# Kernel tuning notes

Measured on AMD Instinct MI355X. Metric: run time of the kernel, lower is better.

The kernel has to match this reference:

```python
import jax, jax.numpy as jnp
import numpy as np

T, D, H = 2048, 1024, 16
HS = D // H  # head_size = 64
DFF = 4 * D
LN_EPS = 1e-6


def layernorm(x, scale, bias, eps=LN_EPS):
    mu = jnp.mean(x, axis=-1, keepdims=True)
    var = jnp.mean(jnp.square(x - mu), axis=-1, keepdims=True)
    return (x - mu) * jax.lax.rsqrt(var + eps) * scale + bias


def setup_inputs() -> dict:
    key = jax.random.key(0)
    ks = jax.random.split(key, 12)
    s_in = 1.0 / np.sqrt(D)
    s_ff = 1.0 / np.sqrt(DFF)
    return {
        "x": jax.random.normal(ks[0], (T, D), jnp.float32),
        "Wq": jax.random.normal(ks[1], (H, D, HS), jnp.float32) * s_in,
        "Wk": jax.random.normal(ks[2], (H, D, HS), jnp.float32) * s_in,
        "Wv": jax.random.normal(ks[3], (H, D, HS), jnp.float32) * s_in,
        "Wo": jax.random.normal(ks[4], (D, D), jnp.float32) * s_in,
        "bo": jnp.zeros((D,), jnp.float32),
        "W1": jax.random.normal(ks[5], (D, DFF), jnp.float32) * s_in,
        "b1": jnp.zeros((DFF,), jnp.float32),
        "W2": jax.random.normal(ks[6], (DFF, D), jnp.float32) * s_ff,
        "b2": jnp.zeros((D,), jnp.float32),
        "ln1_scale": jnp.ones((D,), jnp.float32),
        "ln1_bias": jnp.zeros((D,), jnp.float32),
        "ln2_scale": jnp.ones((D,), jnp.float32),
        "ln2_bias": jnp.zeros((D,), jnp.float32),
        "training": 0,
    }


def reference(x, Wq, Wk, Wv, Wo, bo, W1, b1, W2, b2,
              ln1_scale, ln1_bias, ln2_scale, ln2_bias, training):
    # --- pre-LN causal multi-head self-attention ---
    h = layernorm(x, ln1_scale, ln1_bias)
    q = jnp.einsum("td,hdk->htk", h, Wq)  # [H,T,HS]
    k = jnp.einsum("td,hdk->htk", h, Wk)
    v = jnp.einsum("td,hdk->htk", h, Wv)
    scores = jnp.einsum("htk,hsk->hts", q, k) / jnp.sqrt(jnp.float32(HS))
    causal = jnp.tril(jnp.ones((T, T), jnp.float32))
    scores = jnp.where(causal == 0, -jnp.inf, scores)
    wei = jax.nn.softmax(scores, axis=-1)
    av = jnp.einsum("hts,hsk->htk", wei, v)          # [H,T,HS]
    av = av.transpose(1, 0, 2).reshape(T, H * HS)    # concat over heads
    x = x + av @ Wo + bo                              # dropout deterministic -> identity
    # --- pre-LN feed-forward ---
    h2 = layernorm(x, ln2_scale, ln2_bias)
    ff = jax.nn.relu(h2 @ W1 + b1) @ W2 + b2
    x = x + ff
    return x
```

## Files before the change

### kernel.cpp

```cpp
#include <hip/hip_runtime.h>
#include <cstdint>


typedef __bf16 bf16;
typedef __bf16 bf16x4 __attribute__((ext_vector_type(4)));
typedef __bf16 bf16x8 __attribute__((ext_vector_type(8)));
typedef float floatx4 __attribute__((ext_vector_type(4)));

__device__ __forceinline__ void ld_g2l(const bf16* g, bf16* l) {
    __builtin_amdgcn_global_load_lds(
        (const __attribute__((address_space(1))) void*)g,
        (__attribute__((address_space(3))) void*)l, 16, 0, 0);
}

__device__ __forceinline__ void ln_row_body(
    const float* __restrict__ x, const float* __restrict__ sc,
    const float* __restrict__ bi, bf16* __restrict__ out,
    int row, int tid, float* wred)
{
    const float4 v = ((const float4*)(x + (size_t)row * 1024))[tid];
    float s1 = v.x + v.y + v.z + v.w;
    float s2 = v.x * v.x + v.y * v.y + v.z * v.z + v.w * v.w;
#pragma unroll
    for (int mm = 1; mm < 64; mm <<= 1) {
        s1 += __shfl_xor(s1, mm);
        s2 += __shfl_xor(s2, mm);
    }
    const int wave = tid >> 6, lane = tid & 63;
    if (lane == 0) { wred[wave] = s1; wred[4 + wave] = s2; }
    __syncthreads();
    s1 = wred[0] + wred[1] + wred[2] + wred[3];
    s2 = wred[4] + wred[5] + wred[6] + wred[7];
    const float mu = s1 * (1.f / 1024.f);
    const float var = fmaxf(s2 * (1.f / 1024.f) - mu * mu, 0.f);
    const float rr = rsqrtf(var + 1e-6f);
    const float4 scv = ((const float4*)sc)[tid];
    const float4 biv = ((const float4*)bi)[tid];
    bf16x4 ov;
    ov[0] = (bf16)((v.x - mu) * rr * scv.x + biv.x);
    ov[1] = (bf16)((v.y - mu) * rr * scv.y + biv.y);
    ov[2] = (bf16)((v.z - mu) * rr * scv.z + biv.z);
    ov[3] = (bf16)((v.w - mu) * rr * scv.w + biv.w);
    *(bf16x4*)(out + (size_t)row * 1024 + tid * 4) = ov;
}

__global__ __launch_bounds__(256) void prep_kernel(
    const float* __restrict__ Wq, const float* __restrict__ Wk,
    const float* __restrict__ Wv, bf16* __restrict__ Wqkvt,
    const float* __restrict__ Wo, bf16* __restrict__ Wot,
    const float* __restrict__ W1, bf16* __restrict__ W1t,
    const float* __restrict__ W2, bf16* __restrict__ W2t,
    const float* __restrict__ x, const float* __restrict__ ln1s,
    const float* __restrict__ ln1b, bf16* __restrict__ hbuf)
{
    __shared__ float tile[64][65];
    __shared__ float wred[8];
    const int b = blockIdx.x;
    const int tid = threadIdx.x;

    if (b >= 3072) {
        ln_row_body(x, ln1s, ln1b, hbuf, b - 3072, tid, wred);
        return;
    }

    const int tx = tid & 63, ty = tid >> 6;
    const float* src; bf16* dst; int R, C, c0, r0;
    if (b < 768) {
        const int sec = b >> 4, ti = b & 15;
        const int m = sec >> 4, h = sec & 15;
        src = (m == 0 ? Wq : (m == 1 ? Wk : Wv)) + h * 65536;
        dst = Wqkvt + m * 1048576 + h * 65536;
        R = 1024; C = 64; c0 = 0; r0 = ti * 64;
    } else if (b < 1024) {
        const int i = b - 768;
        src = Wo; dst = Wot; R = 1024; C = 1024;
        c0 = (i & 15) * 64; r0 = (i >> 4) * 64;
    } else if (b < 2048) {
        const int i = b - 1024;
        src = W1; dst = W1t; R = 1024; C = 4096;
        c0 = (i & 63) * 64; r0 = (i >> 6) * 64;
    } else {
        const int i = b - 2048;
        src = W2; dst = W2t; R = 4096; C = 1024;
        c0 = (i & 15) * 64; r0 = (i >> 4) * 64;
    }
#pragma unroll
    for (int i = ty; i < 64; i += 4)
        tile[i][tx] = src[(size_t)(r0 + i) * C + c0 + tx];
    __syncthreads();
#pragma unroll
    for (int i = ty; i < 64; i += 4)
        dst[(size_t)(c0 + i) * R + r0 + tx] = (bf16)tile[tx][i];
}

__global__ __launch_bounds__(256) void ln_kernel(
    const float* __restrict__ x, const float* __restrict__ sc,
    const float* __restrict__ bi, bf16* __restrict__ out)
{
    __shared__ float wred[8];
    ln_row_body(x, sc, bi, out, blockIdx.x, threadIdx.x, wred);
}

__global__ __launch_bounds__(256) void reduce4_kernel(
    const float* __restrict__ p, const float* __restrict__ bias,
    const float* __restrict__ res, float* __restrict__ out)
{
    const int idx = blockIdx.x * 256 + threadIdx.x;
    const int c4 = idx & 255;
    const float4 a0 = ((const float4*)p)[idx];
    const float4 a1 = ((const float4*)(p + 2097152))[idx];
    const float4 a2 = ((const float4*)(p + 4194304))[idx];
    const float4 a3 = ((const float4*)(p + 6291456))[idx];
    const float4 bi = ((const float4*)bias)[c4];
    const float4 r = ((const float4*)res)[idx];
    float4 o;
    o.x = (a0.x + a1.x) + (a2.x + a3.x) + bi.x + r.x;
    o.y = (a0.y + a1.y) + (a2.y + a3.y) + bi.y + r.y;
    o.z = (a0.z + a1.z) + (a2.z + a3.z) + bi.z + r.z;
    o.w = (a0.w + a1.w) + (a2.w + a3.w) + bi.w + r.w;
    ((float4*)out)[idx] = o;
}

template <int MODE, int NG, int MG, int SPLITK>
__global__ __launch_bounds__(512) void gemm128_kernel(
    const bf16* __restrict__ A, const bf16* __restrict__ Bt,
    int N, int K,
    float* __restrict__ outF, bf16* __restrict__ outB,
    const float* __restrict__ bias)
{
    __shared__ __align__(16) bf16 Alds[2][128][64];
    __shared__ __align__(16) bf16 Blds[2][128][64];
    const int tid  = threadIdx.x;
    const int lane = tid & 63;
    const int w    = tid >> 6;
    const int r15  = lane & 15;
    const int quad = lane >> 4;

    const int id    = blockIdx.x + gridDim.x * (blockIdx.y + gridDim.y * blockIdx.z);
    const int xcd   = id & 7;
    const int seq   = id >> 3;
    const int nPerX = gridDim.x / NG;
    const int mPerX = gridDim.y / MG;
    const int nm    = nPerX * mPerX;
    const int z     = seq / nm;
    const int loc   = seq - z * nm;
    const int bn    = ((xcd % NG) * nPerX + (loc % nPerX)) * 128;
    const int bm    = ((xcd / NG) * mPerX + (loc / nPerX)) * 128;

    const int wm = (w >> 2) * 64;
    const int wn = (w & 3) * 32;

    floatx4 acc[4][2];
#pragma unroll
    for (int i = 0; i < 4; ++i)
#pragma unroll
        for (int j = 0; j < 2; ++j) acc[i][j] = (floatx4)(0.f);

    const int KS    = K / SPLITK;
    const int kBase = (SPLITK > 1) ? z * KS : 0;
    const int nIter = KS / 64;

    const int lrow = lane >> 3;
    const int gch  = (lane & 7) ^ lrow;
    const bf16* aptr = A + (size_t)(bm + w * 16 + lrow) * K + kBase + gch * 8;
    const bf16* bptr = Bt + (size_t)(bn + w * 16 + lrow) * K + kBase + gch * 8;

#pragma unroll
    for (int t = 0; t < 2; ++t) {
        ld_g2l(aptr + (size_t)(t * 8) * K, &Alds[0][w * 16 + t * 8][0]);
        ld_g2l(bptr + (size_t)(t * 8) * K, &Blds[0][w * 16 + t * 8][0]);
    }

    for (int it = 0; it < nIter; ++it) {
        const int buf = it & 1;
        __syncthreads();
        if (it + 1 < nIter) {
            const int k2 = (it + 1) * 64;
#pragma unroll
            for (int t = 0; t < 2; ++t) {
                ld_g2l(aptr + (size_t)(t * 8) * K + k2, &Alds[buf ^ 1][w * 16 + t * 8][0]);
                ld_g2l(bptr + (size_t)(t * 8) * K + k2, &Blds[buf ^ 1][w * 16 + t * 8][0]);
            }
        }
#pragma unroll
        for (int kk = 0; kk < 2; ++kk) {
            const int pc = ((kk * 4 + quad) ^ (r15 & 7)) * 8;
            bf16x8 af[4], bfr[2];
#pragma unroll
            for (int i = 0; i < 4; ++i)
                af[i] = *(const bf16x8*)(&Alds[buf][wm + i * 16 + r15][pc]);
#pragma unroll
            for (int j = 0; j < 2; ++j)
                bfr[j] = *(const bf16x8*)(&Blds[buf][wn + j * 16 + r15][pc]);
#pragma unroll
            for (int i = 0; i < 4; ++i)
#pragma unroll
                for (int j = 0; j < 2; ++j)
                    acc[i][j] = __builtin_amdgcn_mfma_f32_16x16x32_bf16(
                        af[i], bfr[j], acc[i][j], 0, 0, 0);
        }
    }

    const int row0 = bm + wm + quad * 4;
    const int col0 = bn + wn + r15;

    if (MODE == 1 && bn >= 2048) {
        bf16* vt = (bf16*)outF;
#pragma unroll
        for (int i = 0; i < 4; ++i) {
            const int row = row0 + i * 16;
#pragma unroll
            for (int j = 0; j < 2; ++j) {
                const int col = col0 + j * 16 - 2048;
                bf16x4 pv;
#pragma unroll
                for (int reg = 0; reg < 4; ++reg) pv[reg] = (bf16)acc[i][j][reg];
                *(bf16x4*)(vt + (size_t)(col >> 6) * 131072
                              + (size_t)(col & 63) * 2048 + row) = pv;
            }
        }
        return;
    }

    float* po = (MODE == 3) ? outF + (size_t)z * 2048 * 1024 : outF;
#pragma unroll
    for (int i = 0; i < 4; ++i) {
#pragma unroll
        for (int reg = 0; reg < 4; ++reg) {
            const int row = row0 + i * 16 + reg;
#pragma unroll
            for (int j = 0; j < 2; ++j) {
                const int col = col0 + j * 16;
                float v = acc[i][j][reg];
                if (MODE == 0 || MODE == 1) {
                    outB[(size_t)row * N + col] = (bf16)v;
                } else if (MODE == 2) {
                    v += bias[col];
                    outB[(size_t)row * N + col] = (bf16)fmaxf(v, 0.f);
                } else {
                    po[(size_t)row * N + col] = v;
                }
            }
        }
    }
}

template <int NG, int MG>
__global__ __launch_bounds__(256) void gemm64_kernel(
    const bf16* __restrict__ A, const bf16* __restrict__ Bt,
    int N, int K,
    float* __restrict__ outF, const float* __restrict__ bias,
    const float* __restrict__ res)
{
    __shared__ __align__(16) bf16 Alds[2][64][64];
    __shared__ __align__(16) bf16 Blds[2][64][64];
    const int tid  = threadIdx.x;
    const int lane = tid & 63;
    const int w    = tid >> 6;
    const int r15  = lane & 15;
    const int quad = lane >> 4;

    const int id    = blockIdx.x + gridDim.x * blockIdx.y;
    const int xcd   = id & 7;
    const int seq   = id >> 3;
    const int nPerX = gridDim.x / NG;
    const int mPerX = gridDim.y / MG;
    const int loc   = seq % (nPerX * mPerX);
    const int bn    = ((xcd % NG) * nPerX + (loc % nPerX)) * 64;
    const int bm    = ((xcd / NG) * mPerX + (loc / nPerX)) * 64;

    const int wm = (w >> 1) * 32;
    const int wn = (w & 1) * 32;

    floatx4 acc[2][2];
#pragma unroll
    for (int i = 0; i < 2; ++i)
#pragma unroll
        for (int j = 0; j < 2; ++j) acc[i][j] = (floatx4)(0.f);

    const int nIter = K / 64;
    const int lrow = lane >> 3;
    const int gch  = (lane & 7) ^ lrow;
    const bf16* aptr = A + (size_t)(bm + w * 16 + lrow) * K + gch * 8;
    const bf16* bptr = Bt + (size_t)(bn + w * 16 + lrow) * K + gch * 8;

#pragma unroll
    for (int t = 0; t < 2; ++t) {
        ld_g2l(aptr + (size_t)t * 8 * K, &Alds[0][w * 16 + t * 8][0]);
        ld_g2l(bptr + (size_t)t * 8 * K, &Blds[0][w * 16 + t * 8][0]);
    }

    for (int it = 0; it < nIter; ++it) {
        const int buf = it & 1;
        __syncthreads();
        if (it + 1 < nIter) {
            const int k2 = (it + 1) * 64;
#pragma unroll
            for (int t = 0; t < 2; ++t) {
                ld_g2l(aptr + (size_t)t * 8 * K + k2, &Alds[buf ^ 1][w * 16 + t * 8][0]);
                ld_g2l(bptr + (size_t)t * 8 * K + k2, &Blds[buf ^ 1][w * 16 + t * 8][0]);
            }
        }
#pragma unroll
        for (int kk = 0; kk < 2; ++kk) {
            const int pc = ((kk * 4 + quad) ^ (r15 & 7)) * 8;
            bf16x8 af[2], bfr[2];
#pragma unroll
            for (int i = 0; i < 2; ++i)
                af[i] = *(const bf16x8*)(&Alds[buf][wm + i * 16 + r15][pc]);
#pragma unroll
            for (int j = 0; j < 2; ++j)
                bfr[j] = *(const bf16x8*)(&Blds[buf][wn + j * 16 + r15][pc]);
#pragma unroll
            for (int i = 0; i < 2; ++i)
#pragma unroll
                for (int j = 0; j < 2; ++j)
                    acc[i][j] = __builtin_amdgcn_mfma_f32_16x16x32_bf16(
                        af[i], bfr[j], acc[i][j], 0, 0, 0);
        }
    }

    const int row0 = bm + wm + quad * 4;
    const int col0 = bn + wn + r15;
#pragma unroll
    for (int i = 0; i < 2; ++i)
#pragma unroll
        for (int reg = 0; reg < 4; ++reg) {
            const int row = row0 + i * 16 + reg;
#pragma unroll
            for (int j = 0; j < 2; ++j) {
                const int col = col0 + j * 16;
                outF[(size_t)row * N + col] =
                    acc[i][j][reg] + bias[col] + res[(size_t)row * N + col];
            }
        }
}

__global__ __launch_bounds__(256) void attn_kernel(
    const bf16* __restrict__ qkv, const bf16* __restrict__ vt,
    bf16* __restrict__ Opart, float* __restrict__ Lpart)
{
    __shared__ __align__(16) bf16 Qs[64][64];
    __shared__ __align__(16) bf16 Ks[2][64][64];
    __shared__ __align__(16) bf16 Vs[2][64][64];
    __shared__ __align__(16) bf16 Ps[4][16][72];

    const int tid  = threadIdx.x;
    const int w    = tid >> 6;
    const int lane = tid & 63;
    const int r15  = lane & 15;
    const int quad = lane >> 4;
    const int rl   = lane >> 3;
    const int gsw  = (lane & 7) ^ (rl & 7);

    const int b    = blockIdx.x;
    const int idp  = b & 255;
    const int seq  = idp >> 3;
    const int h    = (idp & 7) * 2 + (seq & 1);
    const int qp   = seq >> 1;
    const int qt   = ((b >> 8) & 1) ? 31 - qp : qp;
    const int half = b >> 9;
    const int qrow0 = qt * 64;

    const int n0    = (qt + 2) >> 1;
    const int sbBeg = half ? n0 : 0;
    const int sbEnd = half ? qt + 1 : n0;

    if (sbBeg >= sbEnd) return;

    const int tile = half * 512 + h * 32 + qt;
    const size_t obase = (size_t)tile * 4096;

    const bf16* qsec = qkv + h * 64;
    const bf16* ksec = qkv + 1024 + h * 64;
    const bf16* vth  = vt + (size_t)h * 64 * 2048;
    const int s0 = sbBeg * 64;

#pragma unroll
    for (int t = 0; t < 2; ++t) {
        const int r = t * 32 + w * 8 + rl;
        ld_g2l(qsec + (size_t)(qrow0 + r) * 3072 + gsw * 8, &Qs[t * 32 + w * 8][0]);
        ld_g2l(ksec + (size_t)(s0 + r) * 3072 + gsw * 8, &Ks[0][t * 32 + w * 8][0]);
        ld_g2l(vth + (size_t)r * 2048 + s0 + gsw * 8, &Vs[0][t * 32 + w * 8][0]);
    }
    __syncthreads();

    bf16x8 qf[2];
#pragma unroll
    for (int c = 0; c < 2; ++c) {
        const int p = ((c * 4 + quad) ^ (r15 & 7)) * 8;
        qf[c] = *(const bf16x8*)&Qs[w * 16 + r15][p];
    }

    float lacc[4] = {0.f, 0.f, 0.f, 0.f};
    floatx4 O[4];
#pragma unroll
    for (int j = 0; j < 4; ++j) O[j] = (floatx4)(0.f);

    int ns = 0;
#pragma unroll 1
    for (int sb = sbBeg; sb < sbEnd; ++sb, ++ns) {
        const int buf = ns & 1;
        if (sb + 1 < sbEnd) {
            const int s1 = (sb + 1) * 64;
#pragma unroll
            for (int t = 0; t < 2; ++t) {
                const int r = t * 32 + w * 8 + rl;
                ld_g2l(ksec + (size_t)(s1 + r) * 3072 + gsw * 8, &Ks[buf ^ 1][t * 32 + w * 8][0]);
                ld_g2l(vth + (size_t)r * 2048 + s1 + gsw * 8, &Vs[buf ^ 1][t * 32 + w * 8][0]);
            }
        }

        floatx4 S[4];
#pragma unroll
        for (int j = 0; j < 4; ++j) S[j] = (floatx4)(0.f);
        __builtin_amdgcn_s_setprio(1);
#pragma unroll
        for (int c = 0; c < 2; ++c) {
#pragma unroll
            for (int j = 0; j < 4; ++j) {
                const int p = ((c * 4 + quad) ^ (r15 & 7)) * 8;
                const bf16x8 kb = *(const bf16x8*)&Ks[buf][j * 16 + r15][p];
                S[j] = __builtin_amdgcn_mfma_f32_16x16x32_bf16(qf[c], kb, S[j], 0, 0, 0);
            }
        }
        __builtin_amdgcn_s_setprio(0);
        if (sb == qt) {
            const int rowl = w * 16 + quad * 4;
#pragma unroll
            for (int j = 0; j < 4; ++j) {
                const int col = j * 16 + r15;
#pragma unroll
                for (int r = 0; r < 4; ++r) {
                    float p = exp2f(fmaf(S[j][r], 0.18033688f, -28.853901f));
                    if (col > rowl + r) p = 0.f;
                    S[j][r] = p;
                    lacc[r] += p;
                }
            }
        } else {
#pragma unroll
            for (int j = 0; j < 4; ++j)
#pragma unroll
                for (int r = 0; r < 4; ++r) {
                    const float p = exp2f(fmaf(S[j][r], 0.18033688f, -28.853901f));
                    S[j][r] = p;
                    lacc[r] += p;
                }
        }
#pragma unroll
        for (int r = 0; r < 4; ++r)
#pragma unroll
            for (int j = 0; j < 4; ++j)
                Ps[w][quad * 4 + r][j * 16 + r15] = (bf16)S[j][r];
        __builtin_amdgcn_s_setprio(1);
#pragma unroll
        for (int c = 0; c < 2; ++c) {
            const bf16x8 a = *(const bf16x8*)&Ps[w][r15][c * 32 + quad * 8];
#pragma unroll
            for (int j = 0; j < 4; ++j) {
                const int p = ((c * 4 + quad) ^ (r15 & 7)) * 8;
                const bf16x8 vb = *(const bf16x8*)&Vs[buf][j * 16 + r15][p];
                O[j] = __builtin_amdgcn_mfma_f32_16x16x32_bf16(a, vb, O[j], 0, 0, 0);
            }
        }
        __builtin_amdgcn_s_setprio(0);
        __syncthreads();
    }
#pragma unroll
    for (int r = 0; r < 4; ++r) {
#pragma unroll
        for (int d = 1; d < 16; d <<= 1) lacc[r] += __shfl_xor(lacc[r], d);
    }
#pragma unroll
    for (int r = 0; r < 4; ++r) {
        const int row = w * 16 + quad * 4 + r;
#pragma unroll
        for (int j = 0; j < 4; ++j)
            Opart[obase + (size_t)row * 64 + j * 16 + r15] = (bf16)(O[j][r]);
    }
    if (r15 == 0) {
#pragma unroll
        for (int r = 0; r < 4; ++r)
            Lpart[tile * 64 + w * 16 + quad * 4 + r] = lacc[r];
    }
}

__global__ __launch_bounds__(256) void attn_combine_kernel(
    const bf16* __restrict__ Op, const float* __restrict__ Lp,
    bf16* __restrict__ out)
{
    const int b = blockIdx.x;
    const int h = b >> 5, qt = b & 31;
    const int tid = threadIdx.x;
    const int r = tid >> 2, cg = tid & 3;
    const size_t pa = (size_t)b * 4096 + r * 64 + cg * 16;
    const bf16x8 a0 = *(const bf16x8*)(Op + pa);
    const bf16x8 a1 = *(const bf16x8*)(Op + pa + 8);
    const float la = Lp[b * 64 + r];
    bf16x8 o0, o1;
    if (qt > 0) {
        const bf16x8 b0 = *(const bf16x8*)(Op + 2097152 + pa);
        const bf16x8 b1 = *(const bf16x8*)(Op + 2097152 + pa + 8);
        const float lb = Lp[32768 + b * 64 + r];
        const float inv = 1.f / (la + lb);
#pragma unroll
        for (int i = 0; i < 8; ++i) {
            o0[i] = (bf16)(((float)a0[i] + (float)b0[i]) * inv);
            o1[i] = (bf16)(((float)a1[i] + (float)b1[i]) * inv);
        }
    } else {
        const float inv = 1.f / la;
#pragma unroll
        for (int i = 0; i < 8; ++i) {
            o0[i] = (bf16)((float)a0[i] * inv);
            o1[i] = (bf16)((float)a1[i] * inv);
        }
    }
    bf16* dst = out + (size_t)(qt * 64 + r) * 1024 + h * 64 + cg * 16;
    *(bf16x8*)dst = o0;
    *(bf16x8*)(dst + 8) = o1;
}

extern "C" void kernel_launch(void* const* d_in, const int* in_sizes, int n_in,
                              void* d_out, int out_size, void* d_ws, size_t ws_size,
                              hipStream_t stream)
{
    const float* x    = (const float*)d_in[0];
    const float* Wq   = (const float*)d_in[1];
    const float* Wk   = (const float*)d_in[2];
    const float* Wv   = (const float*)d_in[3];
    const float* Wo   = (const float*)d_in[4];
    const float* bo   = (const float*)d_in[5];
    const float* W1   = (const float*)d_in[6];
    const float* b1   = (const float*)d_in[7];
    const float* W2   = (const float*)d_in[8];
    const float* b2   = (const float*)d_in[9];
    const float* ln1s = (const float*)d_in[10];
    const float* ln1b = (const float*)d_in[11];
    const float* ln2s = (const float*)d_in[12];
    const float* ln2b = (const float*)d_in[13];

    char* ws = (char*)d_ws;
    bf16*  Wqkvt = (bf16*)(ws + 0);
    bf16*  Wot   = (bf16*)(ws + 6291456);
    bf16*  W1t   = (bf16*)(ws + 8388608);
    bf16*  W2t   = (bf16*)(ws + 16777216);
    bf16*  hbuf  = (bf16*)(ws + 25165824);
    bf16*  QKV   = (bf16*)(ws + 29360128);
    bf16*  Vt    = (bf16*)(ws + 41943040);
    bf16*  Obuf  = (bf16*)(ws + 46137344);
    float* x1    = (float*)(ws + 50331648);
    bf16*  h2    = (bf16*)(ws + 58720256);
    bf16*  ff1   = (bf16*)(ws + 62914560);
    float* psum  = (float*)(ws + 79691776);
    bf16*  Opart = (bf16*)(ws + 79691776);
    float* Lpart = (float*)(ws + 88080384);

    prep_kernel<<<5120, 256, 0, stream>>>(Wq, Wk, Wv, Wqkvt, Wo, Wot,
                                          W1, W1t, W2, W2t,
                                          x, ln1s, ln1b, hbuf);
    gemm128_kernel<1,4,2,1><<<dim3(24, 16), 512, 0, stream>>>(hbuf, Wqkvt, 3072, 1024, (float*)Vt, QKV, nullptr);
    attn_kernel<<<1024, 256, 0, stream>>>(QKV, Vt, Opart, Lpart);
    attn_combine_kernel<<<512, 256, 0, stream>>>(Opart, Lpart, Obuf);
    gemm64_kernel<4,2><<<dim3(16, 32), 256, 0, stream>>>(Obuf, Wot, 1024, 1024, x1, bo, x);
    ln_kernel<<<2048, 256, 0, stream>>>(x1, ln2s, ln2b, h2);
    gemm128_kernel<2,4,2,1><<<dim3(32, 16), 512, 0, stream>>>(h2, W1t, 4096, 1024, nullptr, ff1, b1);
    gemm128_kernel<3,2,4,4><<<dim3(8, 16, 4), 512, 0, stream>>>(ff1, W2t, 1024, 4096, psum, nullptr, nullptr);
    reduce4_kernel<<<2048, 256, 0, stream>>>(psum, b2, x1, (float*)d_out);
}
```

Measured before the change: 248.1 us.

## Fuse attention split combine into O-projection GEMM and store split-K partials as bf16

Removes the separate attention-combine kernel and has the O-projection GEMM load the two partial attention outputs and their normalizers directly, normalizing them in registers before writing the A tile into LDS. The next tile's partials are prefetched through registers while the current tile's MFMAs run. Separately, the FFN down-projection now writes its split-K partials as bf16 instead of fp32, halving that traffic, and the reduce kernel handles 8 elements per thread. The cost is extra register pressure and VALU work inside the GEMM loop, plus extra rounding of the partial sums before they are reduced.

```diff
diff --git a/kernel.cpp b/kernel.cpp
--- a/kernel.cpp
+++ b/kernel.cpp
@@ -102,23 +102,31 @@
 }
 
 __global__ __launch_bounds__(256) void reduce4_kernel(
-    const float* __restrict__ p, const float* __restrict__ bias,
+    const bf16* __restrict__ p, const float* __restrict__ bias,
     const float* __restrict__ res, float* __restrict__ out)
 {
     const int idx = blockIdx.x * 256 + threadIdx.x;
-    const int c4 = idx & 255;
-    const float4 a0 = ((const float4*)p)[idx];
-    const float4 a1 = ((const float4*)(p + 2097152))[idx];
-    const float4 a2 = ((const float4*)(p + 4194304))[idx];
-    const float4 a3 = ((const float4*)(p + 6291456))[idx];
-    const float4 bi = ((const float4*)bias)[c4];
-    const float4 r = ((const float4*)res)[idx];
-    float4 o;
-    o.x = (a0.x + a1.x) + (a2.x + a3.x) + bi.x + r.x;
-    o.y = (a0.y + a1.y) + (a2.y + a3.y) + bi.y + r.y;
-    o.z = (a0.z + a1.z) + (a2.z + a3.z) + bi.z + r.z;
-    o.w = (a0.w + a1.w) + (a2.w + a3.w) + bi.w + r.w;
-    ((float4*)out)[idx] = o;
+    const size_t e = (size_t)idx * 8;
+    const int c = (int)(e & 1023);
+    const bf16x8 a0 = *(const bf16x8*)(p + e);
+    const bf16x8 a1 = *(const bf16x8*)(p + 2097152 + e);
+    const bf16x8 a2 = *(const bf16x8*)(p + 4194304 + e);
+    const bf16x8 a3 = *(const bf16x8*)(p + 6291456 + e);
+    const float4 b0 = *(const float4*)(bias + c);
+    const float4 b1 = *(const float4*)(bias + c + 4);
+    const float4 r0 = *(const float4*)(res + e);
+    const float4 r1 = *(const float4*)(res + e + 4);
+    float o[8];
+#pragma unroll
+    for (int i = 0; i < 8; ++i)
+        o[i] = ((float)a0[i] + (float)a1[i]) + ((float)a2[i] + (float)a3[i]);
+    float4 o0, o1;
+    o0.x = o[0] + b0.x + r0.x; o0.y = o[1] + b0.y + r0.y;
+    o0.z = o[2] + b0.z + r0.z; o0.w = o[3] + b0.w + r0.w;
+    o1.x = o[4] + b1.x + r1.x; o1.y = o[5] + b1.y + r1.y;
+    o1.z = o[6] + b1.z + r1.z; o1.w = o[7] + b1.w + r1.w;
+    *(float4*)(out + e) = o0;
+    *(float4*)(out + e + 4) = o1;
 }
 
 template <int MODE, int NG, int MG, int SPLITK>
@@ -222,7 +230,7 @@
         return;
     }
 
-    float* po = (MODE == 3) ? outF + (size_t)z * 2048 * 1024 : outF;
+    bf16* po = (MODE == 3) ? outB + (size_t)z * 2097152 : outB;
 #pragma unroll
     for (int i = 0; i < 4; ++i) {
 #pragma unroll
@@ -238,7 +246,7 @@
                     v += bias[col];
                     outB[(size_t)row * N + col] = (bf16)fmaxf(v, 0.f);
                 } else {
-                    po[(size_t)row * N + col] = v;
+                    po[(size_t)row * N + col] = (bf16)v;
                 }
             }
         }
@@ -246,12 +254,13 @@
 }
 
 template <int NG, int MG>
-__global__ __launch_bounds__(256) void gemm64_kernel(
-    const bf16* __restrict__ A, const bf16* __restrict__ Bt,
-    int N, int K,
+__global__ __launch_bounds__(256) void oproj_kernel(
+    const bf16* __restrict__ Opart, const float* __restrict__ Lpart,
+    const bf16* __restrict__ Bt,
     float* __restrict__ outF, const float* __restrict__ bias,
     const float* __restrict__ res)
 {
+    const int N = 1024, K = 1024;
     __shared__ __align__(16) bf16 Alds[2][64][64];
     __shared__ __align__(16) bf16 Blds[2][64][64];
     const int tid  = threadIdx.x;
@@ -271,6 +280,8 @@
 
     const int wm = (w >> 1) * 32;
     const int wn = (w & 1) * 32;
+    const int qt = bm >> 6;
+    const bool hasB = (qt > 0);
 
     floatx4 acc[2][2];
 #pragma unroll
@@ -281,24 +292,63 @@
     const int nIter = K / 64;
     const int lrow = lane >> 3;
     const int gch  = (lane & 7) ^ lrow;
-    const bf16* aptr = A + (size_t)(bm + w * 16 + lrow) * K + gch * 8;
     const bf16* bptr = Bt + (size_t)(bn + w * 16 + lrow) * K + gch * 8;
 
-#pragma unroll
-    for (int t = 0; t < 2; ++t) {
-        ld_g2l(aptr + (size_t)t * 8 * K, &Alds[0][w * 16 + t * 8][0]);
-        ld_g2l(bptr + (size_t)t * 8 * K, &Blds[0][w * 16 + t * 8][0]);
+    const int rit0 = w * 16 + lrow;
+    const int rit1 = rit0 + 8;
+
+#pragma unroll
+    for (int t = 0; t < 2; ++t)
+        ld_g2l(bptr + (size_t)(t * 8) * K, &Blds[0][w * 16 + t * 8][0]);
+    {
+        const size_t tb = (size_t)qt * 4096;
+#pragma unroll
+        for (int t = 0; t < 2; ++t) {
+            const int rit = t ? rit1 : rit0;
+            const size_t off = tb + (size_t)rit * 64 + gch * 8;
+            const bf16x8 a = *(const bf16x8*)(Opart + off);
+            float la = Lpart[qt * 64 + rit];
+            bf16x8 bv; float lb = 0.f;
+#pragma unroll
+            for (int i = 0; i < 8; ++i) bv[i] = (bf16)0.f;
+            if (hasB) {
+                bv = *(const bf16x8*)(Opart + 2097152 + off);
+                lb = Lpart[32768 + qt * 64 + rit];
+            }
+            const float inv = 1.f / (la + lb);
+            bf16x8 o;
+#pragma unroll
+            for (int i = 0; i < 8; ++i)
+                o[i] = (bf16)(((float)a[i] + (float)bv[i]) * inv);
+            *(bf16x8*)(&Alds[0][w * 16 + t * 8 + lrow][(lane & 7) * 8]) = o;
+        }
     }
 
     for (int it = 0; it < nIter; ++it) {
         const int buf = it & 1;
         __syncthreads();
-        if (it + 1 < nIter) {
+        bf16x8 na[2], nb[2];
+        float nla[2], nlb[2];
+        const bool pf = (it + 1 < nIter);
+        if (pf) {
             const int k2 = (it + 1) * 64;
 #pragma unroll
+            for (int t = 0; t < 2; ++t)
+                ld_g2l(bptr + (size_t)(t * 8) * K + k2, &Blds[buf ^ 1][w * 16 + t * 8][0]);
+            const size_t tb = (size_t)((it + 1) * 32 + qt) * 4096;
+#pragma unroll
             for (int t = 0; t < 2; ++t) {
-                ld_g2l(aptr + (size_t)t * 8 * K + k2, &Alds[buf ^ 1][w * 16 + t * 8][0]);
-                ld_g2l(bptr + (size_t)t * 8 * K + k2, &Blds[buf ^ 1][w * 16 + t * 8][0]);
+                const int rit = t ? rit1 : rit0;
+                const size_t off = tb + (size_t)rit * 64 + gch * 8;
+                na[t] = *(const bf16x8*)(Opart + off);
+                nla[t] = Lpart[((it + 1) * 32 + qt) * 64 + rit];
+#pragma unroll
+                for (int i = 0; i < 8; ++i) nb[t][i] = (bf16)0.f;
+                nlb[t] = 0.f;
+                if (hasB) {
+                    nb[t] = *(const bf16x8*)(Opart + 2097152 + off);
+                    nlb[t] = Lpart[32768 + ((it + 1) * 32 + qt) * 64 + rit];
+                }
             }
         }
 #pragma unroll
@@ -317,6 +367,17 @@
                 for (int j = 0; j < 2; ++j)
                     acc[i][j] = __builtin_amdgcn_mfma_f32_16x16x32_bf16(
                         af[i], bfr[j], acc[i][j], 0, 0, 0);
+        }
+        if (pf) {
+#pragma unroll
+            for (int t = 0; t < 2; ++t) {
+                const float inv = 1.f / (nla[t] + nlb[t]);
+                bf16x8 o;
+#pragma unroll
+                for (int i = 0; i < 8; ++i)
+                    o[i] = (bf16)(((float)na[t][i] + (float)nb[t][i]) * inv);
+                *(bf16x8*)(&Alds[buf ^ 1][w * 16 + t * 8 + lrow][(lane & 7) * 8]) = o;
+            }
         }
     }
 
@@ -484,42 +545,6 @@
         for (int r = 0; r < 4; ++r)
             Lpart[tile * 64 + w * 16 + quad * 4 + r] = lacc[r];
     }
-}
-
-__global__ __launch_bounds__(256) void attn_combine_kernel(
-    const bf16* __restrict__ Op, const float* __restrict__ Lp,
-    bf16* __restrict__ out)
-{
-    const int b = blockIdx.x;
-    const int h = b >> 5, qt = b & 31;
-    const int tid = threadIdx.x;
-    const int r = tid >> 2, cg = tid & 3;
-    const size_t pa = (size_t)b * 4096 + r * 64 + cg * 16;
-    const bf16x8 a0 = *(const bf16x8*)(Op + pa);
-    const bf16x8 a1 = *(const bf16x8*)(Op + pa + 8);
-    const float la = Lp[b * 64 + r];
-    bf16x8 o0, o1;
-    if (qt > 0) {
-        const bf16x8 b0 = *(const bf16x8*)(Op + 2097152 + pa);
-        const bf16x8 b1 = *(const bf16x8*)(Op + 2097152 + pa + 8);
-        const float lb = Lp[32768 + b * 64 + r];
-        const float inv = 1.f / (la + lb);
-#pragma unroll
-        for (int i = 0; i < 8; ++i) {
-            o0[i] = (bf16)(((float)a0[i] + (float)b0[i]) * inv);
-            o1[i] = (bf16)(((float)a1[i] + (float)b1[i]) * inv);
-        }
-    } else {
-        const float inv = 1.f / la;
-#pragma unroll
-        for (int i = 0; i < 8; ++i) {
-            o0[i] = (bf16)((float)a0[i] * inv);
-            o1[i] = (bf16)((float)a1[i] * inv);
-        }
-    }
-    bf16* dst = out + (size_t)(qt * 64 + r) * 1024 + h * 64 + cg * 16;
-    *(bf16x8*)dst = o0;
-    *(bf16x8*)(dst + 8) = o1;
 }
 
 extern "C" void kernel_launch(void* const* d_in, const int* in_sizes, int n_in,
@@ -549,23 +574,21 @@
     bf16*  hbuf  = (bf16*)(ws + 25165824);
     bf16*  QKV   = (bf16*)(ws + 29360128);
     bf16*  Vt    = (bf16*)(ws + 41943040);
-    bf16*  Obuf  = (bf16*)(ws + 46137344);
     float* x1    = (float*)(ws + 50331648);
     bf16*  h2    = (bf16*)(ws + 58720256);
     bf16*  ff1   = (bf16*)(ws + 62914560);
-    float* psum  = (float*)(ws + 79691776);
+    bf16*  psum  = (bf16*)(ws + 79691776);
     bf16*  Opart = (bf16*)(ws + 79691776);
-    float* Lpart = (float*)(ws + 88080384);
+    float* Lpart = (float*)(ws + 96468992);
 
     prep_kernel<<<5120, 256, 0, stream>>>(Wq, Wk, Wv, Wqkvt, Wo, Wot,
                                           W1, W1t, W2, W2t,
                                           x, ln1s, ln1b, hbuf);
     gemm128_kernel<1,4,2,1><<<dim3(24, 16), 512, 0, stream>>>(hbuf, Wqkvt, 3072, 1024, (float*)Vt, QKV, nullptr);
     attn_kernel<<<1024, 256, 0, stream>>>(QKV, Vt, Opart, Lpart);
-    attn_combine_kernel<<<512, 256, 0, stream>>>(Opart, Lpart, Obuf);
-    gemm64_kernel<4,2><<<dim3(16, 32), 256, 0, stream>>>(Obuf, Wot, 1024, 1024, x1, bo, x);
+    oproj_kernel<4,2><<<dim3(16, 32), 256, 0, stream>>>(Opart, Lpart, Wot, x1, bo, x);
     ln_kernel<<<2048, 256, 0, stream>>>(x1, ln2s, ln2b, h2);
     gemm128_kernel<2,4,2,1><<<dim3(32, 16), 512, 0, stream>>>(h2, W1t, 4096, 1024, nullptr, ff1, b1);
-    gemm128_kernel<3,2,4,4><<<dim3(8, 16, 4), 512, 0, stream>>>(ff1, W2t, 1024, 4096, psum, nullptr, nullptr);
-    reduce4_kernel<<<2048, 256, 0, stream>>>(psum, b2, x1, (float*)d_out);
-}
+    gemm128_kernel<3,2,4,4><<<dim3(8, 16, 4), 512, 0, stream>>>(ff1, W2t, 1024, 4096, nullptr, psum, nullptr);
+    reduce4_kernel<<<1024, 256, 0, stream>>>(psum, b2, x1, (float*)d_out);
+}
```

Result: no change. 246.3 us (-0.7%).
